# Kernel tuning notes

Hardware: AMD Instinct MI355X
Metric: run time of the kernel (lower is better)

Reference implementation:

```python
import jax, jax.numpy as jnp
import numpy as np


def _tanh_approx(x):
    return x * jax.lax.rsqrt(1.0 + x * x)


def _lru(u, nu_log, gamma_log, Bm, Cm, Dv):
    # u: [B,T,H]; nu_log/gamma_log: [N]; Bm: [N,H]; Cm: [H,N]; Dv: [H]
    A = jnp.exp(-jnp.exp(nu_log))                       # [N], |A|<1
    Bu = jnp.exp(gamma_log) * jnp.einsum('bth,nh->btn', u, Bm)  # [B,T,N]
    A_full = jnp.broadcast_to(A, Bu.shape)
    # diagonal linear recurrence h_t = A*h_{t-1} + Bu_t via parallel scan
    def comb(c1, c2):
        a1, b1 = c1
        a2, b2 = c2
        return (a1 * a2, a2 * b1 + b2)
    _, h = jax.lax.associative_scan(comb, (A_full, Bu), axis=1)  # inclusive scan
    # module uses the state delayed by one step (out[0]=0, out[t]=h_{t-1})
    h_prev = jnp.pad(h[:, :-1, :], ((0, 0), (1, 0), (0, 0)))
    y = jnp.einsum('btn,hn->bth', h_prev, Cm) + Dv * u
    return y


def _model_block(x, nu_log, gamma_log, Bm, Cm, Dv, Wlin, blin):
    y = _lru(x, nu_log, gamma_log, Bm, Cm, Dv)
    y = _tanh_approx(y) @ Wlin.T + blin
    return y + x


def setup_inputs() -> dict:
    key = jax.random.key(0)
    ks = jax.random.split(key, 10)
    B_, T_, N, H, D = 16, 65536, 64, 64, 4
    r_min, r_max = 0.8, 1.0
    u = jax.random.uniform(ks[0], (D, N))
    nu_log = jnp.log(-0.5 * jnp.log(u * (r_max ** 2 - r_min ** 2) + r_min ** 2))
    A = jnp.exp(-jnp.exp(nu_log))
    gamma_log = jnp.log(jnp.sqrt(1.0 - A ** 2))
    Bm = jax.random.normal(ks[1], (D, N, H)) / np.sqrt(2.0 * H)
    Cm = jax.random.normal(ks[2], (D, H, N)) / np.sqrt(N)
    Dv = jax.random.normal(ks[3], (D, H))
    Wlin = jax.random.normal(ks[4], (D, H, H)) / np.sqrt(H)
    blin = jnp.zeros((D, H))
    Win = jax.random.normal(ks[5], (H, 1))
    Wout = jax.random.normal(ks[6], (1, H)) / np.sqrt(H)
    x = jax.random.normal(ks[7], (B_, T_, 1))
    return {"x": x, "Win": Win, "nu_log": nu_log, "gamma_log": gamma_log,
            "Bm": Bm, "Cm": Cm, "Dv": Dv, "Wlin": Wlin, "blin": blin, "Wout": Wout}


def reference(x, Win, nu_log, gamma_log, Bm, Cm, Dv, Wlin, blin, Wout):
    h = x @ Win.T  # [B,T,H]
    depth = nu_log.shape[0]
    for i in range(depth):
        h = _model_block(h, nu_log[i], gamma_log[i], Bm[i], Cm[i], Dv[i], Wlin[i], blin[i])
    return h @ Wout.T  # [B,T,1]
```

## Files before the change

kernel.cpp:

```cpp
#include <hip/hip_runtime.h>

#define B_ 16
#define T_ 65536
#define H_ 64
#define DEPTH_ 4
#define CHUNK 128
#define NCH (T_ / CHUNK)

typedef _Float16 f16;
typedef f16 f16x8 __attribute__((ext_vector_type(8)));
typedef float f32x4 __attribute__((ext_vector_type(4)));
typedef unsigned u32x4 __attribute__((ext_vector_type(4)));

#define MFMA(a, b, c) __builtin_amdgcn_mfma_f32_16x16x32_f16(a, b, c, 0, 0, 0)
#define SWZ(t, k) ((t) * 64 + ((k) ^ (((t) & 7) << 2)))

union U4F8 { u32x4 u; f16x8 h; };

__device__ __forceinline__ f16x8 ldfrag(const f16* p) { return *(const f16x8*)p; }

__global__ __launch_bounds__(256)
void prep(const float* __restrict__ Win, const float* __restrict__ nu,
          const float* __restrict__ ga, const float* __restrict__ Bm,
          const float* __restrict__ Cm, const float* __restrict__ Dv,
          const float* __restrict__ Wl,
          f16* __restrict__ BmH, f16* __restrict__ BmL,
          f16* __restrict__ CmH, f16* __restrict__ CmL,
          f16* __restrict__ WlH, float* __restrict__ atab, float* __restrict__ sc)
{
    const int tid = threadIdx.x;
    for (int l = 0; l < DEPTH_; ++l) {
        for (int idx = tid; idx < 4096; idx += 256) {
            int n = idx >> 6;
            float g = expf(ga[l * 64 + n]);
            float v = Bm[l * 4096 + idx] * g;
            f16 h = (f16)v;
            BmH[l * 4096 + idx] = h;
            BmL[l * 4096 + idx] = (f16)(v - (float)h);
            float cv = Cm[l * 4096 + idx];
            h = (f16)cv;
            CmH[l * 4096 + idx] = h;
            CmL[l * 4096 + idx] = (f16)(cv - (float)h);
            WlH[l * 4096 + idx] = (f16)Wl[l * 4096 + idx];
        }
        if (tid < 64) {
            int n = tid;
            float ex = expf(nu[l * 64 + n]);
            float a = expf(-ex);
            float g = expf(ga[l * 64 + n]);
            sc[l * 320 + n] = a;
            sc[l * 320 + 64 + n] = Dv[l * 64 + n];
            float bw = 0.f;
            for (int h2 = 0; h2 < 64; ++h2) bw += Bm[l * 4096 + n * 64 + h2] * Win[h2];
            sc[l * 320 + 128 + n] = bw * g;
            sc[l * 320 + 192 + n] = Dv[l * 64 + n] * Win[n];
            sc[l * 320 + 256 + n] = Win[n];
        }
        for (int idx = tid; idx < 8192; idx += 256) {
            int n = idx >> 7, j = idx & 127;
            float ex = expf(nu[l * 64 + n]);
            atab[l * 8192 + idx] = expf(-ex * (float)j);
        }
    }
}

__global__ __launch_bounds__(64)
void carry_x(const float* __restrict__ x, const float* __restrict__ sc0,
             float* __restrict__ carry)
{
    const int blk = blockIdx.x;
    const int b = blk >> 9, c = blk & (NCH - 1);
    const int n = threadIdx.x;
    const float a  = sc0[n];
    const float bw = sc0[128 + n];
    __shared__ float xs[64];
    const float* xp = x + (size_t)b * T_ + c * CHUNK;
    float s = 0.f;
    for (int bb = 0; bb < CHUNK / 64; ++bb) {
        __syncthreads();
        xs[n] = xp[bb * 64 + n];
        __syncthreads();
        #pragma unroll
        for (int tt = 0; tt < 64; ++tt) s = a * s + bw * xs[tt];
    }
    carry[((size_t)b * NCH + c) * 64 + n] = s;
}

__global__ __launch_bounds__(256)
void scan_carry(const float* __restrict__ nu_log, float* __restrict__ carry)
{
    const int b = blockIdx.x;
    const int tid = threadIdx.x;
    const int n = tid & 63, q = tid >> 6;
    const float ex = expf(nu_log[n]);
    const float aL = expf(-ex * (float)CHUNK);
    float* cp = carry + (size_t)b * NCH * 64 + n;
    __shared__ float part[4][64];

    const int SEG = NCH / 4;
    const int base = q * SEG;
    float p = 0.f;
    #pragma unroll 4
    for (int i = 0; i < SEG; ++i) {
        float v = cp[(size_t)(base + i) * 64];
        cp[(size_t)(base + i) * 64] = p;
        p = aL * p + v;
    }
    part[q][n] = p;
    __syncthreads();
    if (q > 0) {
        const float aLS = expf(-ex * (float)(CHUNK * SEG));
        float inc = 0.f;
        for (int qq = 0; qq < q; ++qq) inc = inc * aLS + part[qq][n];
        float qv = inc;
        #pragma unroll 4
        for (int i = 0; i < SEG; ++i) {
            cp[(size_t)(base + i) * 64] += qv;
            qv *= aL;
        }
    }
}

struct LPrep {
    const f16 *BmH, *BmL, *CmH, *CmL, *WlH;
    const float *av, *dvv, *bw, *dwin, *win;
    const f16 *BmHn, *BmLn;
    const float *atabn;
    const float *blin, *Wout;
};

template<int IN_X, int OUT_FINAL>
__global__ __launch_bounds__(256, 4)
void lru_fused(const float* __restrict__ x, f16* __restrict__ ubuf,
               LPrep P, float* __restrict__ carry, float* __restrict__ out)
{
    const int blk = blockIdx.x;
    const int b = blk >> 9, c = blk & (NCH - 1);
    const int t0 = c * CHUNK;
    const int tid = threadIdx.x;
    const int w = tid >> 6, lane = tid & 63;
    const int l15 = lane & 15, lq = lane >> 4;

    __shared__ float hpk[CHUNK * 64];
    __shared__ float swv[4][64];
    __shared__ float red[4][64];

    f16* ug = ubuf + ((size_t)b * T_ + t0) * 64;
    const float* xg = x + (size_t)b * T_ + t0;

    f16x8 ahu[2][2];
    if (!IN_X) {
        #pragma unroll
        for (int tt = 0; tt < 2; ++tt) {
            const f16* p = ug + (size_t)((2 * w + tt) * 16 + l15) * 64;
            U4F8 r0, r1;
            r0.u = __builtin_nontemporal_load((const u32x4*)(p + lq * 8));
            r1.u = __builtin_nontemporal_load((const u32x4*)(p + 32 + lq * 8));
            ahu[tt][0] = r0.h;
            ahu[tt][1] = r1.h;
        }
    }

    float av4[4];
    #pragma unroll
    for (int nt = 0; nt < 4; ++nt) av4[nt] = P.av[nt * 16 + l15];

    float xv[2][4];
    if (IN_X) {
        #pragma unroll
        for (int tt = 0; tt < 2; ++tt)
            #pragma unroll
            for (int r = 0; r < 4; ++r)
                xv[tt][r] = xg[32 * w + 16 * tt + 4 * lq + r];
    }

    f32x4 acc[4][2];
    if (IN_X) {
        #pragma unroll
        for (int nt = 0; nt < 4; ++nt) {
            float bwn = P.bw[nt * 16 + l15];
            #pragma unroll
            for (int tt = 0; tt < 2; ++tt)
                #pragma unroll
                for (int r = 0; r < 4; ++r) acc[nt][tt][r] = xv[tt][r] * bwn;
        }
    } else {
        #pragma unroll
        for (int nt = 0; nt < 4; ++nt) {
            int n = nt * 16 + l15;
            f16x8 bh0 = ldfrag(P.BmH + n * 64 + lq * 8);
            f16x8 bh1 = ldfrag(P.BmH + n * 64 + 32 + lq * 8);
            f16x8 bl0 = ldfrag(P.BmL + n * 64 + lq * 8);
            f16x8 bl1 = ldfrag(P.BmL + n * 64 + 32 + lq * 8);
            #pragma unroll
            for (int tt = 0; tt < 2; ++tt) {
                f32x4 a4v = {0.f, 0.f, 0.f, 0.f};
                a4v = MFMA(ahu[tt][0], bh0, a4v);
                a4v = MFMA(ahu[tt][0], bl0, a4v);
                a4v = MFMA(ahu[tt][1], bh1, a4v);
                a4v = MFMA(ahu[tt][1], bl1, a4v);
                acc[nt][tt] = a4v;
            }
        }
    }

    float Wb[4][2];
    #pragma unroll
    for (int nt = 0; nt < 4; ++nt) {
        float a = av4[nt], a2 = a * a, a4 = a2 * a2, a8 = a4 * a4, a16 = a8 * a8;
        float P0incl = 0.f;
        #pragma unroll
        for (int tt = 0; tt < 2; ++tt) {
            f32x4 xs = acc[nt][tt];
            float L0 = xs[0];
            float L1 = a * L0 + xs[1];
            float L2 = a * L1 + xs[2];
            float Cv = a * L2 + xs[3];
            float u1 = __shfl_up(Cv, 16);
            float t1 = Cv + ((lq >= 1) ? a4 * u1 : 0.f);
            float u2 = __shfl_up(t1, 32);
            float Pv = t1 + ((lq >= 2) ? a8 * u2 : 0.f);
            float E = __shfl_up(Pv, 16);
            E = (lq == 0) ? 0.f : E;
            if (tt == 0) { Wb[nt][0] = E; P0incl = Pv; }
            else {
                float B0 = __shfl(P0incl, 48 + l15);
                float a4lq = 1.f;
                if (lq & 1) a4lq *= a4;
                if (lq & 2) a4lq *= a8;
                Wb[nt][1] = E + a4lq * B0;
                if (lq == 3) swv[w][nt * 16 + l15] = Pv + a16 * B0;
            }
        }
    }
    __syncthreads();

    #pragma unroll
    for (int nt = 0; nt < 4; ++nt) {
        int n = nt * 16 + l15;
        float a = av4[nt], a2 = a * a, a4 = a2 * a2, a8 = a4 * a4, a16 = a8 * a8, a32 = a16 * a16;
        float inc = carry[((size_t)b * NCH + c) * 64 + n];
        for (int ww = 0; ww < w; ++ww) inc = inc * a32 + swv[ww][n];
        float a4lq = 1.f;
        if (lq & 1) a4lq *= a4;
        if (lq & 2) a4lq *= a8;
        #pragma unroll
        for (int tt = 0; tt < 2; ++tt) {
            float Z = Wb[nt][tt] + a4lq * (tt ? a16 : 1.f) * inc;
            float s = Z;
            #pragma unroll
            for (int r = 0; r < 4; ++r) {
                int t = 32 * w + 16 * tt + 4 * lq + r;
                hpk[SWZ(t, n)] = s;
                s = a * s + acc[nt][tt][r];
            }
        }
    }

    #pragma unroll
    for (int tt = 0; tt < 2; ++tt) {
        int tb = 2 * w + tt, trow = tb * 16 + l15, sw = (trow & 7) << 2;
        const float* hw = hpk + trow * 64;
        f16x8 ah[2], al[2];
        #pragma unroll
        for (int kk = 0; kk < 2; ++kk) {
            int kb = kk * 32 + lq * 8;
            float4 v0 = *(const float4*)(hw + (kb ^ sw));
            float4 v1 = *(const float4*)(hw + ((kb + 4) ^ sw));
            float vv[8] = {v0.x, v0.y, v0.z, v0.w, v1.x, v1.y, v1.z, v1.w};
            #pragma unroll
            for (int i = 0; i < 8; ++i) {
                f16 h = (f16)vv[i];
                ah[kk][i] = h;
                al[kk][i] = (f16)(vv[i] - (float)h);
            }
        }
        #pragma unroll
        for (int nt = 0; nt < 4; ++nt) {
            int n = nt * 16 + l15;
            f16x8 ch0 = ldfrag(P.CmH + n * 64 + lq * 8);
            f16x8 ch1 = ldfrag(P.CmH + n * 64 + 32 + lq * 8);
            f16x8 cl0 = ldfrag(P.CmL + n * 64 + lq * 8);
            f16x8 cl1 = ldfrag(P.CmL + n * 64 + 32 + lq * 8);
            f32x4 a4v = {0.f, 0.f, 0.f, 0.f};
            a4v = MFMA(ah[0], ch0, a4v);
            a4v = MFMA(al[0], ch0, a4v);
            a4v = MFMA(ah[0], cl0, a4v);
            a4v = MFMA(ah[1], ch1, a4v);
            a4v = MFMA(al[1], ch1, a4v);
            a4v = MFMA(ah[1], cl1, a4v);
            if (!IN_X) {
                float dv = P.dvv[n];
                f16 dh = (f16)dv, dl = (f16)(dv - (float)dh);
                f16x8 dfh, dfl;
                #pragma unroll
                for (int i2 = 0; i2 < 8; ++i2) { dfh[i2] = (f16)0.f; dfl[i2] = (f16)0.f; }
                int e = ((nt & 1) * 16 + l15) - lq * 8;
                if (e >= 0 && e < 8) { dfh[e] = dh; dfl[e] = dl; }
                a4v = MFMA(ahu[tt][nt >> 1], dfh, a4v);
                a4v = MFMA(ahu[tt][nt >> 1], dfl, a4v);
            }
            float dwin = IN_X ? P.dwin[n] : 0.f;
            #pragma unroll
            for (int r = 0; r < 4; ++r) {
                int t = tb * 16 + lq * 4 + r;
                float y = a4v[r];
                if (IN_X) y += xv[tt][r] * dwin;
                hpk[SWZ(t, n)] = y * rsqrtf(1.f + y * y);
            }
        }
    }

    f16* stg = (f16*)hpk;
    #pragma unroll
    for (int tt = 0; tt < 2; ++tt) {
        int tb = 2 * w + tt, trow = tb * 16 + l15, sw = (trow & 7) << 2;
        const float* hw = hpk + trow * 64;
        f16x8 t0f, t1f;
        #pragma unroll
        for (int kk = 0; kk < 2; ++kk) {
            int kb = kk * 32 + lq * 8;
            float4 v0 = *(const float4*)(hw + (kb ^ sw));
            float4 v1 = *(const float4*)(hw + ((kb + 4) ^ sw));
            float vv[8] = {v0.x, v0.y, v0.z, v0.w, v1.x, v1.y, v1.z, v1.w};
            #pragma unroll
            for (int i = 0; i < 8; ++i) {
                if (kk == 0) t0f[i] = (f16)vv[i]; else t1f[i] = (f16)vv[i];
            }
        }
        float val[4] = {0.f, 0.f, 0.f, 0.f};
        #pragma unroll
        for (int nt = 0; nt < 4; ++nt) {
            int n = nt * 16 + l15;
            f16x8 w0f = ldfrag(P.WlH + n * 64 + lq * 8);
            f16x8 w1f = ldfrag(P.WlH + n * 64 + 32 + lq * 8);
            f32x4 a4v = {0.f, 0.f, 0.f, 0.f};
            a4v = MFMA(t0f, w0f, a4v);
            a4v = MFMA(t1f, w1f, a4v);
            if (!IN_X) {
                f16x8 ifr;
                #pragma unroll
                for (int i2 = 0; i2 < 8; ++i2) ifr[i2] = (f16)0.f;
                int e = ((nt & 1) * 16 + l15) - lq * 8;
                if (e >= 0 && e < 8) ifr[e] = (f16)1.f;
                a4v = MFMA(ahu[tt][nt >> 1], ifr, a4v);
            }
            float blj = P.blin[n];
            float wij = IN_X ? P.win[n] : 0.f;
            float woj = OUT_FINAL ? P.Wout[n] : 0.f;
            #pragma unroll
            for (int r = 0; r < 4; ++r) {
                int t = tb * 16 + lq * 4 + r;
                float o = a4v[r] + blj;
                if (IN_X) o += xv[tt][r] * wij;
                if (OUT_FINAL) {
                    val[r] += o * woj;
                } else {
                    int g = n >> 1;
                    int word = t * 64 + (((g & ~3) ^ ((t & 7) << 2)) | (g & 3));
                    stg[word * 2 + (n & 1)] = (f16)o;
                }
            }
        }
        if (OUT_FINAL) {
            #pragma unroll
            for (int r = 0; r < 4; ++r) {
                float p = val[r];
                p += __shfl_xor(p, 1);
                p += __shfl_xor(p, 2);
                p += __shfl_xor(p, 4);
                p += __shfl_xor(p, 8);
                if (l15 == 0) out[(size_t)b * T_ + t0 + tb * 16 + lq * 4 + r] = p;
            }
        }
    }

    if (!OUT_FINAL) {
        #pragma unroll
        for (int i = 0; i < 4; ++i) {
            int row = 32 * w + i * 8 + (lane >> 3);
            int gg = 4 * (lane & 7);
            int word = row * 64 + (gg ^ ((row & 7) << 2));
            u32x4 cv = *(const u32x4*)(hpk + word);
            __builtin_nontemporal_store(cv, (u32x4*)(ug + (size_t)row * 64 + 8 * (lane & 7)));
        }

        float partial[4] = {0.f, 0.f, 0.f, 0.f};
        #pragma unroll
        for (int tt = 0; tt < 2; ++tt) {
            int tb = 2 * w + tt, arow = tb * 16 + l15, msk = (arow & 7) << 2;
            U4F8 av0, av1;
            av0.u = *(const u32x4*)(hpk + arow * 64 + ((4 * lq) ^ msk));
            av1.u = *(const u32x4*)(hpk + arow * 64 + ((16 + 4 * lq) ^ msk));
            #pragma unroll
            for (int nt = 0; nt < 4; ++nt) {
                int n = nt * 16 + l15;
                f16x8 bh0 = ldfrag(P.BmHn + n * 64 + lq * 8);
                f16x8 bh1 = ldfrag(P.BmHn + n * 64 + 32 + lq * 8);
                f16x8 bl0 = ldfrag(P.BmLn + n * 64 + lq * 8);
                f16x8 bl1 = ldfrag(P.BmLn + n * 64 + 32 + lq * 8);
                f32x4 a4v = {0.f, 0.f, 0.f, 0.f};
                a4v = MFMA(av0.h, bh0, a4v);
                a4v = MFMA(av0.h, bl0, a4v);
                a4v = MFMA(av1.h, bh1, a4v);
                a4v = MFMA(av1.h, bl1, a4v);
                float4 dp = *(const float4*)(P.atabn + n * 128 + 124 - tb * 16 - lq * 4);
                partial[nt] += a4v[0] * dp.w + a4v[1] * dp.z + a4v[2] * dp.y + a4v[3] * dp.x;
            }
        }
        #pragma unroll
        for (int nt = 0; nt < 4; ++nt) {
            float v = partial[nt];
            v += __shfl_xor(v, 16);
            v += __shfl_xor(v, 32);
            if (lq == 0) red[w][nt * 16 + l15] = v;
        }
        __syncthreads();
        if (w == 0)
            carry[((size_t)b * NCH + c) * 64 + lane] =
                red[0][lane] + red[1][lane] + red[2][lane] + red[3][lane];
    }
}

extern "C" void kernel_launch(void* const* d_in, const int* in_sizes, int n_in,
                              void* d_out, int out_size, void* d_ws, size_t ws_size,
                              hipStream_t stream)
{
    const float* x   = (const float*)d_in[0];
    const float* Win = (const float*)d_in[1];
    const float* nu  = (const float*)d_in[2];
    const float* ga  = (const float*)d_in[3];
    const float* Bm  = (const float*)d_in[4];
    const float* Cm  = (const float*)d_in[5];
    const float* Dv  = (const float*)d_in[6];
    const float* Wl  = (const float*)d_in[7];
    const float* bl  = (const float*)d_in[8];
    const float* Wo  = (const float*)d_in[9];
    float* out = (float*)d_out;

    char* p = (char*)d_ws;
    f16* ubuf = (f16*)p;            p += (size_t)B_ * T_ * 64 * sizeof(f16);
    float* carry = (float*)p;       p += (size_t)B_ * NCH * 64 * sizeof(float);
    f16* wBmH = (f16*)p;            p += 4 * 4096 * sizeof(f16);
    f16* wBmL = (f16*)p;            p += 4 * 4096 * sizeof(f16);
    f16* wCmH = (f16*)p;            p += 4 * 4096 * sizeof(f16);
    f16* wCmL = (f16*)p;            p += 4 * 4096 * sizeof(f16);
    f16* wWlH = (f16*)p;            p += 4 * 4096 * sizeof(f16);
    float* atab = (float*)p;        p += 4 * 8192 * sizeof(float);
    float* sc = (float*)p;          p += 4 * 320 * sizeof(float);

    dim3 grid(B_ * NCH), blk256(256), blk64(64), gscan(B_);

    prep<<<1, 256, 0, stream>>>(Win, nu, ga, Bm, Cm, Dv, Wl,
                                wBmH, wBmL, wCmH, wCmL, wWlH, atab, sc);
    carry_x<<<grid, blk64, 0, stream>>>(x, sc, carry);

    for (int l = 0; l < DEPTH_; ++l) {
        int ln = (l + 1 < DEPTH_) ? l + 1 : l;
        scan_carry<<<gscan, blk256, 0, stream>>>(nu + l * 64, carry);
        LPrep Pr;
        Pr.BmH = wBmH + l * 4096;  Pr.BmL = wBmL + l * 4096;
        Pr.CmH = wCmH + l * 4096;  Pr.CmL = wCmL + l * 4096;
        Pr.WlH = wWlH + l * 4096;
        Pr.av = sc + l * 320;       Pr.dvv = sc + l * 320 + 64;
        Pr.bw = sc + l * 320 + 128; Pr.dwin = sc + l * 320 + 192;
        Pr.win = sc + l * 320 + 256;
        Pr.BmHn = wBmH + ln * 4096; Pr.BmLn = wBmL + ln * 4096;
        Pr.atabn = atab + ln * 8192;
        Pr.blin = bl + l * 64; Pr.Wout = Wo;
        if (l == 0)
            lru_fused<1, 0><<<grid, blk256, 0, stream>>>(x, ubuf, Pr, carry, out);
        else if (l == DEPTH_ - 1)
            lru_fused<0, 1><<<grid, blk256, 0, stream>>>(x, ubuf, Pr, carry, out);
        else
            lru_fused<0, 0><<<grid, blk256, 0, stream>>>(x, ubuf, Pr, carry, out);
    }
}
```

Measured before the change: 1.410 ms.

## Halve scan chunk to 64, precompute diagonal fragments, batch carry scan loads

Reduces the chunk length from 128 to 64 so each wave handles one 16-row tile, which doubles the block count and raises the launch-bounds occupancy hint from 4 to 8 blocks per SM. The Dv-diagonal and identity MFMA fragments are now precomputed in prep and loaded, instead of being built per thread. carry_x is restructured to one wave per chunk using shuffles, and scan_carry loads in batches of 8 to overlap latency. The trade-off is twice as many chunk carries, which lengthens the sequential carry scan.

Result: slower. 1.979 ms (+40.4%).

```diff
diff --git a/kernel.cpp b/kernel.cpp
--- a/kernel.cpp
+++ b/kernel.cpp
@@ -4,7 +4,7 @@
 #define T_ 65536
 #define H_ 64
 #define DEPTH_ 4
-#define CHUNK 128
+#define CHUNK 64
 #define NCH (T_ / CHUNK)
 
 typedef _Float16 f16;
@@ -26,7 +26,8 @@
           const float* __restrict__ Wl,
           f16* __restrict__ BmH, f16* __restrict__ BmL,
           f16* __restrict__ CmH, f16* __restrict__ CmL,
-          f16* __restrict__ WlH, float* __restrict__ atab, float* __restrict__ sc)
+          f16* __restrict__ WlH, float* __restrict__ atab, float* __restrict__ sc,
+          f16* __restrict__ dvfH, f16* __restrict__ dvfL, f16* __restrict__ idf)
 {
     const int tid = threadIdx.x;
     for (int l = 0; l < DEPTH_; ++l) {
@@ -56,34 +57,46 @@
             sc[l * 320 + 192 + n] = Dv[l * 64 + n] * Win[n];
             sc[l * 320 + 256 + n] = Win[n];
         }
-        for (int idx = tid; idx < 8192; idx += 256) {
-            int n = idx >> 7, j = idx & 127;
+        for (int idx = tid; idx < 4096; idx += 256) {
+            int n = idx >> 6, j = idx & 63;
             float ex = expf(nu[l * 64 + n]);
-            atab[l * 8192 + idx] = expf(-ex * (float)j);
-        }
+            atab[l * 4096 + idx] = expf(-ex * (float)j);
+        }
+        for (int idx = tid; idx < 2048; idx += 256) {
+            int nt = idx >> 9, lane = (idx >> 3) & 63, j = idx & 7;
+            int l15 = lane & 15, lq = lane >> 4;
+            int e = ((nt & 1) * 16 + l15) - lq * 8;
+            int n = nt * 16 + l15;
+            float val = (j == e) ? Dv[l * 64 + n] : 0.f;
+            f16 h = (f16)val;
+            dvfH[l * 2048 + idx] = h;
+            dvfL[l * 2048 + idx] = (f16)(val - (float)h);
+        }
+    }
+    for (int idx = tid; idx < 2048; idx += 256) {
+        int nt = idx >> 9, lane = (idx >> 3) & 63, j = idx & 7;
+        int l15 = lane & 15, lq = lane >> 4;
+        int e = ((nt & 1) * 16 + l15) - lq * 8;
+        idf[idx] = (j == e) ? (f16)1.f : (f16)0.f;
     }
 }
 
-__global__ __launch_bounds__(64)
+__global__ __launch_bounds__(256)
 void carry_x(const float* __restrict__ x, const float* __restrict__ sc0,
              float* __restrict__ carry)
 {
     const int blk = blockIdx.x;
-    const int b = blk >> 9, c = blk & (NCH - 1);
-    const int n = threadIdx.x;
-    const float a  = sc0[n];
-    const float bw = sc0[128 + n];
-    __shared__ float xs[64];
-    const float* xp = x + (size_t)b * T_ + c * CHUNK;
+    const int b = blk >> 8;
+    const int tid = threadIdx.x;
+    const int w = tid >> 6, lane = tid & 63;
+    const int c = (blk & 255) * 4 + w;
+    const float a  = sc0[lane];
+    const float bw = sc0[128 + lane];
+    float xval = x[(size_t)b * T_ + (size_t)c * CHUNK + lane];
     float s = 0.f;
-    for (int bb = 0; bb < CHUNK / 64; ++bb) {
-        __syncthreads();
-        xs[n] = xp[bb * 64 + n];
-        __syncthreads();
-        #pragma unroll
-        for (int tt = 0; tt < 64; ++tt) s = a * s + bw * xs[tt];
-    }
-    carry[((size_t)b * NCH + c) * 64 + n] = s;
+    #pragma unroll
+    for (int t = 0; t < 64; ++t) s = a * s + bw * __shfl(xval, t);
+    carry[((size_t)b * NCH + c) * 64 + lane] = s;
 }
 
 __global__ __launch_bounds__(256)
@@ -100,11 +113,22 @@
     const int SEG = NCH / 4;
     const int base = q * SEG;
     float p = 0.f;
-    #pragma unroll 4
-    for (int i = 0; i < SEG; ++i) {
-        float v = cp[(size_t)(base + i) * 64];
-        cp[(size_t)(base + i) * 64] = p;
-        p = aL * p + v;
+    float v[8], nv[8];
+    #pragma unroll
+    for (int j = 0; j < 8; ++j) v[j] = cp[(size_t)(base + j) * 64];
+    for (int i0 = 0; i0 < SEG; i0 += 8) {
+        if (i0 + 8 < SEG) {
+            #pragma unroll
+            for (int j = 0; j < 8; ++j) nv[j] = cp[(size_t)(base + i0 + 8 + j) * 64];
+        }
+        #pragma unroll
+        for (int j = 0; j < 8; ++j) {
+            float vv = v[j];
+            cp[(size_t)(base + i0 + j) * 64] = p;
+            p = aL * p + vv;
+        }
+        #pragma unroll
+        for (int j = 0; j < 8; ++j) v[j] = nv[j];
     }
     part[q][n] = p;
     __syncthreads();
@@ -112,30 +136,37 @@
         const float aLS = expf(-ex * (float)(CHUNK * SEG));
         float inc = 0.f;
         for (int qq = 0; qq < q; ++qq) inc = inc * aLS + part[qq][n];
-        float qv = inc;
-        #pragma unroll 4
-        for (int i = 0; i < SEG; ++i) {
-            cp[(size_t)(base + i) * 64] += qv;
-            qv *= aL;
+        for (int i0 = 0; i0 < SEG; i0 += 8) {
+            float qs = inc;
+            float o[8];
+            #pragma unroll
+            for (int j = 0; j < 8; ++j) { o[j] = cp[(size_t)(base + i0 + j) * 64]; }
+            #pragma unroll
+            for (int j = 0; j < 8; ++j) {
+                cp[(size_t)(base + i0 + j) * 64] = o[j] + qs;
+                qs *= aL;
+            }
+            inc = qs;
         }
     }
 }
 
 struct LPrep {
     const f16 *BmH, *BmL, *CmH, *CmL, *WlH;
-    const float *av, *dvv, *bw, *dwin, *win;
+    const float *av, *bw, *dwin, *win;
+    const f16 *dvfH, *dvfL, *idf;
     const f16 *BmHn, *BmLn;
     const float *atabn;
     const float *blin, *Wout;
 };
 
 template<int IN_X, int OUT_FINAL>
-__global__ __launch_bounds__(256, 4)
+__global__ __launch_bounds__(256, 8)
 void lru_fused(const float* __restrict__ x, f16* __restrict__ ubuf,
                LPrep P, float* __restrict__ carry, float* __restrict__ out)
 {
     const int blk = blockIdx.x;
-    const int b = blk >> 9, c = blk & (NCH - 1);
+    const int b = blk >> 10, c = blk & (NCH - 1);
     const int t0 = c * CHUNK;
     const int tid = threadIdx.x;
     const int w = tid >> 6, lane = tid & 63;
@@ -148,41 +179,38 @@
     f16* ug = ubuf + ((size_t)b * T_ + t0) * 64;
     const float* xg = x + (size_t)b * T_ + t0;
 
-    f16x8 ahu[2][2];
+    const int trow = w * 16 + l15;
+
+    f16x8 ahu[2];
     if (!IN_X) {
-        #pragma unroll
-        for (int tt = 0; tt < 2; ++tt) {
-            const f16* p = ug + (size_t)((2 * w + tt) * 16 + l15) * 64;
-            U4F8 r0, r1;
-            r0.u = __builtin_nontemporal_load((const u32x4*)(p + lq * 8));
-            r1.u = __builtin_nontemporal_load((const u32x4*)(p + 32 + lq * 8));
-            ahu[tt][0] = r0.h;
-            ahu[tt][1] = r1.h;
-        }
-    }
-
-    float av4[4];
+        const f16* p = ug + (size_t)trow * 64;
+        U4F8 r0, r1;
+        r0.u = __builtin_nontemporal_load((const u32x4*)(p + lq * 8));
+        r1.u = __builtin_nontemporal_load((const u32x4*)(p + 32 + lq * 8));
+        ahu[0] = r0.h;
+        ahu[1] = r1.h;
+    }
+
+    float av4[4], carr4[4];
     #pragma unroll
-    for (int nt = 0; nt < 4; ++nt) av4[nt] = P.av[nt * 16 + l15];
-
-    float xv[2][4];
+    for (int nt = 0; nt < 4; ++nt) {
+        av4[nt] = P.av[nt * 16 + l15];
+        carr4[nt] = carry[((size_t)b * NCH + c) * 64 + nt * 16 + l15];
+    }
+
+    float xv[4];
     if (IN_X) {
         #pragma unroll
-        for (int tt = 0; tt < 2; ++tt)
-            #pragma unroll
-            for (int r = 0; r < 4; ++r)
-                xv[tt][r] = xg[32 * w + 16 * tt + 4 * lq + r];
-    }
-
-    f32x4 acc[4][2];
+        for (int r = 0; r < 4; ++r) xv[r] = xg[w * 16 + lq * 4 + r];
+    }
+
+    f32x4 acc[4];
     if (IN_X) {
         #pragma unroll
         for (int nt = 0; nt < 4; ++nt) {
             float bwn = P.bw[nt * 16 + l15];
             #pragma unroll
-            for (int tt = 0; tt < 2; ++tt)
-                #pragma unroll
-                for (int r = 0; r < 4; ++r) acc[nt][tt][r] = xv[tt][r] * bwn;
+            for (int r = 0; r < 4; ++r) acc[nt][r] = xv[r] * bwn;
         }
     } else {
         #pragma unroll
@@ -192,74 +220,53 @@
             f16x8 bh1 = ldfrag(P.BmH + n * 64 + 32 + lq * 8);
             f16x8 bl0 = ldfrag(P.BmL + n * 64 + lq * 8);
             f16x8 bl1 = ldfrag(P.BmL + n * 64 + 32 + lq * 8);
-            #pragma unroll
-            for (int tt = 0; tt < 2; ++tt) {
-                f32x4 a4v = {0.f, 0.f, 0.f, 0.f};
-                a4v = MFMA(ahu[tt][0], bh0, a4v);
-                a4v = MFMA(ahu[tt][0], bl0, a4v);
-                a4v = MFMA(ahu[tt][1], bh1, a4v);
-                a4v = MFMA(ahu[tt][1], bl1, a4v);
-                acc[nt][tt] = a4v;
-            }
-        }
-    }
-
-    float Wb[4][2];
+            f32x4 a4v = {0.f, 0.f, 0.f, 0.f};
+            a4v = MFMA(ahu[0], bh0, a4v);
+            a4v = MFMA(ahu[0], bl0, a4v);
+            a4v = MFMA(ahu[1], bh1, a4v);
+            a4v = MFMA(ahu[1], bl1, a4v);
+            acc[nt] = a4v;
+        }
+    }
+
+    float Wb[4];
     #pragma unroll
     for (int nt = 0; nt < 4; ++nt) {
-        float a = av4[nt], a2 = a * a, a4 = a2 * a2, a8 = a4 * a4, a16 = a8 * a8;
-        float P0incl = 0.f;
-        #pragma unroll
-        for (int tt = 0; tt < 2; ++tt) {
-            f32x4 xs = acc[nt][tt];
-            float L0 = xs[0];
-            float L1 = a * L0 + xs[1];
-            float L2 = a * L1 + xs[2];
-            float Cv = a * L2 + xs[3];
-            float u1 = __shfl_up(Cv, 16);
-            float t1 = Cv + ((lq >= 1) ? a4 * u1 : 0.f);
-            float u2 = __shfl_up(t1, 32);
-            float Pv = t1 + ((lq >= 2) ? a8 * u2 : 0.f);
-            float E = __shfl_up(Pv, 16);
-            E = (lq == 0) ? 0.f : E;
-            if (tt == 0) { Wb[nt][0] = E; P0incl = Pv; }
-            else {
-                float B0 = __shfl(P0incl, 48 + l15);
-                float a4lq = 1.f;
-                if (lq & 1) a4lq *= a4;
-                if (lq & 2) a4lq *= a8;
-                Wb[nt][1] = E + a4lq * B0;
-                if (lq == 3) swv[w][nt * 16 + l15] = Pv + a16 * B0;
-            }
-        }
+        float a = av4[nt], a2 = a * a, a4 = a2 * a2, a8 = a4 * a4;
+        f32x4 xs = acc[nt];
+        float L1 = a * xs[0] + xs[1];
+        float L2 = a * L1 + xs[2];
+        float Cv = a * L2 + xs[3];
+        float u1 = __shfl_up(Cv, 16);
+        float t1 = Cv + ((lq >= 1) ? a4 * u1 : 0.f);
+        float u2 = __shfl_up(t1, 32);
+        float Pv = t1 + ((lq >= 2) ? a8 * u2 : 0.f);
+        float E = __shfl_up(Pv, 16);
+        Wb[nt] = (lq == 0) ? 0.f : E;
+        if (lq == 3) swv[w][nt * 16 + l15] = Pv;
     }
     __syncthreads();
 
     #pragma unroll
     for (int nt = 0; nt < 4; ++nt) {
         int n = nt * 16 + l15;
-        float a = av4[nt], a2 = a * a, a4 = a2 * a2, a8 = a4 * a4, a16 = a8 * a8, a32 = a16 * a16;
-        float inc = carry[((size_t)b * NCH + c) * 64 + n];
-        for (int ww = 0; ww < w; ++ww) inc = inc * a32 + swv[ww][n];
+        float a = av4[nt], a2 = a * a, a4 = a2 * a2, a8 = a4 * a4, a16 = a8 * a8;
+        float inc = carr4[nt];
+        for (int ww = 0; ww < w; ++ww) inc = inc * a16 + swv[ww][n];
         float a4lq = 1.f;
         if (lq & 1) a4lq *= a4;
         if (lq & 2) a4lq *= a8;
-        #pragma unroll
-        for (int tt = 0; tt < 2; ++tt) {
-            float Z = Wb[nt][tt] + a4lq * (tt ? a16 : 1.f) * inc;
-            float s = Z;
-            #pragma unroll
-            for (int r = 0; r < 4; ++r) {
-                int t = 32 * w + 16 * tt + 4 * lq + r;
-                hpk[SWZ(t, n)] = s;
-                s = a * s + acc[nt][tt][r];
-            }
-        }
-    }
-
-    #pragma unroll
-    for (int tt = 0; tt < 2; ++tt) {
-        int tb = 2 * w + tt, trow = tb * 16 + l15, sw = (trow & 7) << 2;
+        float s = Wb[nt] + a4lq * inc;
+        #pragma unroll
+        for (int r = 0; r < 4; ++r) {
+            int t = 16 * w + 4 * lq + r;
+            hpk[SWZ(t, n)] = s;
+            s = a * s + acc[nt][r];
+        }
+    }
+
+    {
+        int sw = (trow & 7) << 2;
         const float* hw = hpk + trow * 64;
         f16x8 ah[2], al[2];
         #pragma unroll
@@ -290,31 +297,25 @@
             a4v = MFMA(al[1], ch1, a4v);
             a4v = MFMA(ah[1], cl1, a4v);
             if (!IN_X) {
-                float dv = P.dvv[n];
-                f16 dh = (f16)dv, dl = (f16)(dv - (float)dh);
-                f16x8 dfh, dfl;
-                #pragma unroll
-                for (int i2 = 0; i2 < 8; ++i2) { dfh[i2] = (f16)0.f; dfl[i2] = (f16)0.f; }
-                int e = ((nt & 1) * 16 + l15) - lq * 8;
-                if (e >= 0 && e < 8) { dfh[e] = dh; dfl[e] = dl; }
-                a4v = MFMA(ahu[tt][nt >> 1], dfh, a4v);
-                a4v = MFMA(ahu[tt][nt >> 1], dfl, a4v);
+                f16x8 dfh = ldfrag(P.dvfH + (nt * 64 + lane) * 8);
+                f16x8 dfl = ldfrag(P.dvfL + (nt * 64 + lane) * 8);
+                a4v = MFMA(ahu[nt >> 1], dfh, a4v);
+                a4v = MFMA(ahu[nt >> 1], dfl, a4v);
             }
             float dwin = IN_X ? P.dwin[n] : 0.f;
             #pragma unroll
             for (int r = 0; r < 4; ++r) {
-                int t = tb * 16 + lq * 4 + r;
+                int t = 16 * w + lq * 4 + r;
                 float y = a4v[r];
-                if (IN_X) y += xv[tt][r] * dwin;
+                if (IN_X) y += xv[r] * dwin;
                 hpk[SWZ(t, n)] = y * rsqrtf(1.f + y * y);
             }
         }
     }
 
     f16* stg = (f16*)hpk;
-    #pragma unroll
-    for (int tt = 0; tt < 2; ++tt) {
-        int tb = 2 * w + tt, trow = tb * 16 + l15, sw = (trow & 7) << 2;
+    {
+        int sw = (trow & 7) << 2;
         const float* hw = hpk + trow * 64;
         f16x8 t0f, t1f;
         #pragma unroll
@@ -338,21 +339,17 @@
             a4v = MFMA(t0f, w0f, a4v);
             a4v = MFMA(t1f, w1f, a4v);
             if (!IN_X) {
-                f16x8 ifr;
-                #pragma unroll
-                for (int i2 = 0; i2 < 8; ++i2) ifr[i2] = (f16)0.f;
-                int e = ((nt & 1) * 16 + l15) - lq * 8;
-                if (e >= 0 && e < 8) ifr[e] = (f16)1.f;
-                a4v = MFMA(ahu[tt][nt >> 1], ifr, a4v);
+                f16x8 ifr = ldfrag(P.idf + (nt * 64 + lane) * 8);
+                a4v = MFMA(ahu[nt >> 1], ifr, a4v);
             }
             float blj = P.blin[n];
             float wij = IN_X ? P.win[n] : 0.f;
             float woj = OUT_FINAL ? P.Wout[n] : 0.f;
             #pragma unroll
             for (int r = 0; r < 4; ++r) {
-                int t = tb * 16 + lq * 4 + r;
+                int t = 16 * w + lq * 4 + r;
                 float o = a4v[r] + blj;
-                if (IN_X) o += xv[tt][r] * wij;
+                if (IN_X) o += xv[r] * wij;
                 if (OUT_FINAL) {
                     val[r] += o * woj;
                 } else {
@@ -370,15 +367,15 @@
                 p += __shfl_xor(p, 2);
                 p += __shfl_xor(p, 4);
                 p += __shfl_xor(p, 8);
-                if (l15 == 0) out[(size_t)b * T_ + t0 + tb * 16 + lq * 4 + r] = p;
+                if (l15 == 0) out[(size_t)b * T_ + t0 + 16 * w + lq * 4 + r] = p;
             }
         }
     }
 
     if (!OUT_FINAL) {
         #pragma unroll
-        for (int i = 0; i < 4; ++i) {
-            int row = 32 * w + i * 8 + (lane >> 3);
+        for (int i = 0; i < 2; ++i) {
+            int row = 16 * w + i * 8 + (lane >> 3);
             int gg = 4 * (lane & 7);
             int word = row * 64 + (gg ^ ((row & 7) << 2));
             u32x4 cv = *(const u32x4*)(hpk + word);
@@ -386,12 +383,11 @@
         }
 
         float partial[4] = {0.f, 0.f, 0.f, 0.f};
-        #pragma unroll
-        for (int tt = 0; tt < 2; ++tt) {
-            int tb = 2 * w + tt, arow = tb * 16 + l15, msk = (arow & 7) << 2;
+        {
+            int msk = (trow & 7) << 2;
             U4F8 av0, av1;
-            av0.u = *(const u32x4*)(hpk + arow * 64 + ((4 * lq) ^ msk));
-            av1.u = *(const u32x4*)(hpk + arow * 64 + ((16 + 4 * lq) ^ msk));
+            av0.u = *(const u32x4*)(hpk + trow * 64 + ((4 * lq) ^ msk));
+            av1.u = *(const u32x4*)(hpk + trow * 64 + ((16 + 4 * lq) ^ msk));
             #pragma unroll
             for (int nt = 0; nt < 4; ++nt) {
                 int n = nt * 16 + l15;
@@ -404,7 +400,7 @@
                 a4v = MFMA(av0.h, bl0, a4v);
                 a4v = MFMA(av1.h, bh1, a4v);
                 a4v = MFMA(av1.h, bl1, a4v);
-                float4 dp = *(const float4*)(P.atabn + n * 128 + 124 - tb * 16 - lq * 4);
+                float4 dp = *(const float4*)(P.atabn + n * 64 + 60 - w * 16 - lq * 4);
                 partial[nt] += a4v[0] * dp.w + a4v[1] * dp.z + a4v[2] * dp.y + a4v[3] * dp.x;
             }
         }
@@ -446,14 +442,17 @@
     f16* wCmH = (f16*)p;            p += 4 * 4096 * sizeof(f16);
     f16* wCmL = (f16*)p;            p += 4 * 4096 * sizeof(f16);
     f16* wWlH = (f16*)p;            p += 4 * 4096 * sizeof(f16);
-    float* atab = (float*)p;        p += 4 * 8192 * sizeof(float);
+    float* atab = (float*)p;        p += 4 * 4096 * sizeof(float);
     float* sc = (float*)p;          p += 4 * 320 * sizeof(float);
-
-    dim3 grid(B_ * NCH), blk256(256), blk64(64), gscan(B_);
+    f16* dvfH = (f16*)p;            p += 4 * 2048 * sizeof(f16);
+    f16* dvfL = (f16*)p;            p += 4 * 2048 * sizeof(f16);
+    f16* idf = (f16*)p;             p += 2048 * sizeof(f16);
+
+    dim3 grid(B_ * NCH), blk256(256), gcx(B_ * NCH / 4), gscan(B_);
 
     prep<<<1, 256, 0, stream>>>(Win, nu, ga, Bm, Cm, Dv, Wl,
-                                wBmH, wBmL, wCmH, wCmL, wWlH, atab, sc);
-    carry_x<<<grid, blk64, 0, stream>>>(x, sc, carry);
+                                wBmH, wBmL, wCmH, wCmL, wWlH, atab, sc, dvfH, dvfL, idf);
+    carry_x<<<gcx, blk256, 0, stream>>>(x, sc, carry);
 
     for (int l = 0; l < DEPTH_; ++l) {
         int ln = (l + 1 < DEPTH_) ? l + 1 : l;
@@ -462,11 +461,12 @@
         Pr.BmH = wBmH + l * 4096;  Pr.BmL = wBmL + l * 4096;
         Pr.CmH = wCmH + l * 4096;  Pr.CmL = wCmL + l * 4096;
         Pr.WlH = wWlH + l * 4096;
-        Pr.av = sc + l * 320;       Pr.dvv = sc + l * 320 + 64;
+        Pr.av = sc + l * 320;
         Pr.bw = sc + l * 320 + 128; Pr.dwin = sc + l * 320 + 192;
         Pr.win = sc + l * 320 + 256;
+        Pr.dvfH = dvfH + l * 2048;  Pr.dvfL = dvfL + l * 2048;  Pr.idf = idf;
         Pr.BmHn = wBmH + ln * 4096; Pr.BmLn = wBmL + ln * 4096;
-        Pr.atabn = atab + ln * 8192;
+        Pr.atabn = atab + ln * 4096;
         Pr.blin = bl + l * 64; Pr.Wout = Wo;
         if (l == 0)
             lru_fused<1, 0><<<grid, blk256, 0, stream>>>(x, ubuf, Pr, carry, out);
```
